# Performance work log

Measured on AMD Instinct MI355X. Metric: run time of the kernel, lower is better.

## Reference

```python
import jax, jax.numpy as jnp
import numpy as np

TOP_K = 2

def setup_inputs() -> dict:
    key = jax.random.key(0)
    k0, k1, k2, k3 = jax.random.split(key, 4)
    B, T, D, F, E = 2, 2048, 1024, 4096, 8
    x = jax.random.normal(k0, (B, T, D), dtype=jnp.float32)
    Wr = jax.random.normal(k1, (E, D), dtype=jnp.float32) * 0.02   # router weight [out=E, in=D]
    W1 = jax.random.normal(k2, (E, F, D), dtype=jnp.float32) * 0.02  # per-expert up-proj [out=F, in=D]
    W2 = jax.random.normal(k3, (E, D, F), dtype=jnp.float32) * 0.02  # per-expert down-proj [out=D, in=F]
    return {"x": x, "Wr": Wr, "W1": W1, "W2": W2}

def reference(x, Wr, W1, W2):
    B, T, D = x.shape
    E = Wr.shape[0]
    N = B * T
    xf = x.reshape(N, D)
    # Router in fp32 on the un-cast activations (as in the torch module).
    logits = xf @ Wr.T                                   # [N, E]
    probs = jax.nn.softmax(logits, axis=-1)
    topk_w, topk_idx = jax.lax.top_k(probs, TOP_K)       # [N, K]
    topk_w = topk_w / jnp.sum(topk_w, axis=-1, keepdims=True)
    # Combine weights scattered into a dense [N, E] dispatch/combine matrix
    # (top_k indices are distinct, so .set is exact).
    combine = jnp.zeros((N, E), dtype=jnp.float32)
    combine = combine.at[jnp.arange(N)[:, None], topk_idx].set(topk_w)
    # Expert FFN runs in bf16 (comm_dtype in the original all-to-all pipeline).
    xb = xf.astype(jnp.bfloat16)
    h = jax.nn.gelu(jnp.einsum('nd,efd->enf', xb, W1.astype(jnp.bfloat16)),
                    approximate=False)                   # [E, N, F]
    yo = jnp.einsum('enf,edf->end', h, W2.astype(jnp.bfloat16))  # [E, N, D]
    # Weighted combine: bf16 expert outputs * fp32 gate weights -> fp32 (torch promotion).
    out = jnp.einsum('end,ne->nd', yo.astype(jnp.float32), combine)
    return out.reshape(B, T, D)
```

## Files before the change

kernel.cpp:

```cpp
#include <hip/hip_runtime.h>
#include <hip/hip_bf16.h>

typedef __attribute__((ext_vector_type(8))) __bf16 bf16x8;
typedef __attribute__((ext_vector_type(4))) float floatx4;

constexpr int N_TOK = 4096;
constexpr int DDIM  = 1024;
constexpr int FDIM  = 4096;
constexpr int NEXP  = 8;
constexpr int NSLOT = 2 * N_TOK;

static __device__ __forceinline__ unsigned short f2bf(float f) {
    union { __hip_bfloat16 h; unsigned short u; } v;
    v.h = __float2bfloat16(f);
    return v.u;
}

__global__ void zero_kernel(float* __restrict__ out, int* __restrict__ counts) {
    size_t i = ((size_t)blockIdx.x * 256 + threadIdx.x) * 4;
    *(float4*)(out + i) = make_float4(0.f, 0.f, 0.f, 0.f);
    if (blockIdx.x == 0 && threadIdx.x < NEXP) counts[threadIdx.x] = 0;
}

__global__ void castN_kernel(const float* __restrict__ src, unsigned short* __restrict__ dst, int n4) {
    int i = blockIdx.x * 256 + threadIdx.x;
    if (i >= n4) return;
    float4 v = *(const float4*)(src + (size_t)i * 4);
    ushort4 o;
    o.x = f2bf(v.x); o.y = f2bf(v.y); o.z = f2bf(v.z); o.w = f2bf(v.w);
    *(ushort4*)(dst + (size_t)i * 4) = o;
}

__global__ void router_kernel(const float* __restrict__ x, const float* __restrict__ Wr,
                              int* __restrict__ te, float* __restrict__ tw,
                              int* __restrict__ counts) {
    __shared__ float wr[NEXP * DDIM];
    const int tid = threadIdx.x;
    for (int i = tid; i < NEXP * DDIM; i += 256) wr[i] = Wr[i];
    __syncthreads();
    const int wave = tid >> 6, lane = tid & 63;
    const int t = blockIdx.x * 4 + wave;

    float xr[16];
    const float* xp = x + (size_t)t * DDIM;
    #pragma unroll
    for (int i = 0; i < 16; i++) xr[i] = xp[lane + 64 * i];

    float logit[NEXP];
    #pragma unroll
    for (int e = 0; e < NEXP; e++) {
        float s = 0.f;
        #pragma unroll
        for (int i = 0; i < 16; i++) s += xr[i] * wr[e * DDIM + lane + 64 * i];
        #pragma unroll
        for (int off = 32; off > 0; off >>= 1) s += __shfl_xor(s, off, 64);
        logit[e] = s;
    }
    if (lane == 0) {
        int i0 = 0; float l0 = logit[0];
        #pragma unroll
        for (int e = 1; e < NEXP; e++) if (logit[e] > l0) { l0 = logit[e]; i0 = e; }
        int i1 = -1; float l1 = -3.0e38f;
        #pragma unroll
        for (int e = 0; e < NEXP; e++) if (e != i0 && logit[e] > l1) { l1 = logit[e]; i1 = e; }
        float p1 = __expf(0.f) * expf(l1 - l0);
        float w0 = 1.f / (1.f + p1);
        float w1 = p1 * w0;
        te[t * 2] = i0; te[t * 2 + 1] = i1;
        tw[t * 2] = w0; tw[t * 2 + 1] = w1;
        atomicAdd(&counts[i0], 1);
        atomicAdd(&counts[i1], 1);
    }
}

__global__ void scan_kernel(const int* __restrict__ counts, int* __restrict__ offsets,
                            int* __restrict__ cursors) {
    if (threadIdx.x == 0) {
        int acc = 0;
        for (int e = 0; e < NEXP; e++) { offsets[e] = acc; acc += counts[e]; }
        offsets[NEXP] = acc;
    }
    if (threadIdx.x < NEXP) cursors[threadIdx.x] = 0;
}

__global__ void scatter_kernel(const int* __restrict__ te, const float* __restrict__ tw,
                               const int* __restrict__ offsets, int* __restrict__ cursors,
                               int* __restrict__ rowid, float* __restrict__ gate) {
    int t = blockIdx.x * 256 + threadIdx.x;
    if (t >= N_TOK) return;
    #pragma unroll
    for (int k = 0; k < 2; k++) {
        int e = te[t * 2 + k];
        int pos = atomicAdd(&cursors[e], 1);
        int slot = offsets[e] + pos;
        rowid[slot] = t;
        gate[slot] = tw[t * 2 + k];
    }
}

template <int K, bool UP, bool BF16W>
__global__ __launch_bounds__(256)
void ffn_gemm(const unsigned short* __restrict__ A,
              const float* __restrict__ Wf,
              const unsigned short* __restrict__ Wb,
              unsigned short* __restrict__ Hout,
              float* __restrict__ out,
              const int* __restrict__ rowid,
              const float* __restrict__ gate,
              const int* __restrict__ offsets) {
    constexpr int BM = 128, BN = 128, BK = 32, LDT = 40;
    constexpr int NOUT = UP ? FDIM : DDIM;

    const int e = blockIdx.z;
    const int seg = offsets[e];
    const int cnt = offsets[e + 1] - seg;
    const int m0 = blockIdx.y * BM;
    if (m0 >= cnt) return;
    const int n0 = blockIdx.x * BN;

    __shared__ __align__(16) unsigned short As[BM * LDT];
    __shared__ __align__(16) unsigned short Bs[BN * LDT];

    const int tid = threadIdx.x;
    const int lane = tid & 63;
    const int wave = tid >> 6;
    const int wm = (wave >> 1) * 64;
    const int wn = (wave & 1) * 64;
    const int frow = lane & 15;
    const int quad = lane >> 4;

    floatx4 acc[4][4];
    #pragma unroll
    for (int i = 0; i < 4; i++)
        #pragma unroll
        for (int j = 0; j < 4; j++)
            acc[i][j] = (floatx4){0.f, 0.f, 0.f, 0.f};

    const int ar = tid >> 1;
    const int ah = (tid & 1) * 16;

    int slotA = seg + m0 + ar;
    if (slotA > NSLOT - 1) slotA = NSLOT - 1;
    const unsigned short* aptr;
    if (UP) aptr = A + (size_t)rowid[slotA] * DDIM + ah;
    else    aptr = A + (size_t)slotA * FDIM + ah;
    unsigned short* asdst = &As[ar * LDT + ah];
    unsigned short* bsdst = &Bs[ar * LDT + ah];
    const float* bptrf = Wf + ((size_t)e * NOUT + n0 + ar) * K + ah;
    const unsigned short* bptrb = Wb + ((size_t)e * NOUT + n0 + ar) * K + ah;

    for (int k0 = 0; k0 < K; k0 += BK) {
        uint4 a0 = *(const uint4*)(aptr);
        uint4 a1 = *(const uint4*)(aptr + 8);
        uint4 bu0, bu1;
        if (BF16W) {
            bu0 = *(const uint4*)(bptrb);
            bu1 = *(const uint4*)(bptrb + 8);
        } else {
            float4 b0 = *(const float4*)(bptrf);
            float4 b1 = *(const float4*)(bptrf + 4);
            float4 b2 = *(const float4*)(bptrf + 8);
            float4 b3 = *(const float4*)(bptrf + 12);
            union { unsigned short u[16]; uint4 q[2]; } bb;
            bb.u[0] = f2bf(b0.x); bb.u[1] = f2bf(b0.y); bb.u[2]  = f2bf(b0.z); bb.u[3]  = f2bf(b0.w);
            bb.u[4] = f2bf(b1.x); bb.u[5] = f2bf(b1.y); bb.u[6]  = f2bf(b1.z); bb.u[7]  = f2bf(b1.w);
            bb.u[8] = f2bf(b2.x); bb.u[9] = f2bf(b2.y); bb.u[10] = f2bf(b2.z); bb.u[11] = f2bf(b2.w);
            bb.u[12] = f2bf(b3.x); bb.u[13] = f2bf(b3.y); bb.u[14] = f2bf(b3.z); bb.u[15] = f2bf(b3.w);
            bu0 = bb.q[0]; bu1 = bb.q[1];
        }
        __syncthreads();
        *(uint4*)(asdst) = a0;
        *(uint4*)(asdst + 8) = a1;
        *(uint4*)(bsdst) = bu0;
        *(uint4*)(bsdst + 8) = bu1;
        __syncthreads();

        bf16x8 av[4], bv[4];
        #pragma unroll
        for (int i = 0; i < 4; i++)
            av[i] = *(const bf16x8*)&As[(wm + i * 16 + frow) * LDT + quad * 8];
        #pragma unroll
        for (int i = 0; i < 4; i++)
            bv[i] = *(const bf16x8*)&Bs[(wn + i * 16 + frow) * LDT + quad * 8];
        #pragma unroll
        for (int mt = 0; mt < 4; mt++)
            #pragma unroll
            for (int nt = 0; nt < 4; nt++)
                acc[mt][nt] = __builtin_amdgcn_mfma_f32_16x16x32_bf16(av[mt], bv[nt], acc[mt][nt], 0, 0, 0);

        aptr += BK;
        if (BF16W) bptrb += BK; else bptrf += BK;
    }

    #pragma unroll
    for (int mt = 0; mt < 4; mt++) {
        #pragma unroll
        for (int r = 0; r < 4; r++) {
            int mloc = m0 + wm + mt * 16 + quad * 4 + r;
            if (mloc >= cnt) continue;
            int slot = seg + mloc;
            if (UP) {
                #pragma unroll
                for (int nt = 0; nt < 4; nt++) {
                    int n = n0 + wn + nt * 16 + frow;
                    float v = acc[mt][nt][r];
                    float g = 0.5f * v * (1.0f + erff(v * 0.70710678118654752f));
                    Hout[(size_t)slot * FDIM + n] = f2bf(g);
                }
            } else {
                int t = rowid[slot];
                float gw = gate[slot];
                #pragma unroll
                for (int nt = 0; nt < 4; nt++) {
                    int n = n0 + wn + nt * 16 + frow;
                    atomicAdd(&out[(size_t)t * DDIM + n], gw * acc[mt][nt][r]);
                }
            }
        }
    }
}

extern "C" void kernel_launch(void* const* d_in, const int* in_sizes, int n_in,
                              void* d_out, int out_size, void* d_ws, size_t ws_size,
                              hipStream_t stream) {
    const float* x  = (const float*)d_in[0];
    const float* Wr = (const float*)d_in[1];
    const float* W1 = (const float*)d_in[2];
    const float* W2 = (const float*)d_in[3];
    float* out = (float*)d_out;

    char* ws = (char*)d_ws;
    size_t off = 0;
    auto alloc = [&](size_t bytes) -> char* {
        char* p = ws + off;
        off = (off + bytes + 255) & ~(size_t)255;
        return p;
    };
    unsigned short* xb   = (unsigned short*)alloc((size_t)N_TOK * DDIM * 2);
    unsigned short* H    = (unsigned short*)alloc((size_t)NSLOT * FDIM * 2);
    int*   rowid   = (int*)alloc(NSLOT * 4);
    float* gatew   = (float*)alloc(NSLOT * 4);
    int*   te      = (int*)alloc(NSLOT * 4);
    float* tw      = (float*)alloc(NSLOT * 4);
    int*   counts  = (int*)alloc(64);
    int*   offsets = (int*)alloc(64);
    int*   cursors = (int*)alloc(64);
    unsigned short* w1b = (unsigned short*)alloc((size_t)NEXP * FDIM * DDIM * 2);
    unsigned short* w2b = (unsigned short*)alloc((size_t)NEXP * DDIM * FDIM * 2);
    const bool bf16w = (off <= ws_size);

    zero_kernel<<<4096, 256, 0, stream>>>(out, counts);
    castN_kernel<<<(N_TOK * DDIM / 4 + 255) / 256, 256, 0, stream>>>(x, xb, N_TOK * DDIM / 4);
    if (bf16w) {
        const int n4 = NEXP * FDIM * DDIM / 4;
        castN_kernel<<<(n4 + 255) / 256, 256, 0, stream>>>(W1, w1b, n4);
        castN_kernel<<<(n4 + 255) / 256, 256, 0, stream>>>(W2, w2b, n4);
    }
    router_kernel<<<N_TOK / 4, 256, 0, stream>>>(x, Wr, te, tw, counts);
    scan_kernel<<<1, 64, 0, stream>>>(counts, offsets, cursors);
    scatter_kernel<<<(N_TOK + 255) / 256, 256, 0, stream>>>(te, tw, offsets, cursors, rowid, gatew);

    if (bf16w) {
        ffn_gemm<DDIM, true,  true ><<<dim3(FDIM / 128, 32, NEXP), 256, 0, stream>>>(xb, W1, w1b, H, out, rowid, gatew, offsets);
        ffn_gemm<FDIM, false, true ><<<dim3(DDIM / 128, 32, NEXP), 256, 0, stream>>>(H,  W2, w2b, H, out, rowid, gatew, offsets);
    } else {
        ffn_gemm<DDIM, true,  false><<<dim3(FDIM / 128, 32, NEXP), 256, 0, stream>>>(xb, W1, w1b, H, out, rowid, gatew, offsets);
        ffn_gemm<FDIM, false, false><<<dim3(DDIM / 128, 32, NEXP), 256, 0, stream>>>(H,  W2, w2b, H, out, rowid, gatew, offsets);
    }
}
```

Measured before the change: 732.0 us.

## Load GEMM tiles with direct global-to-LDS and replace atomic combine with slot buffer

```diff
diff --git a/kernel.cpp b/kernel.cpp
--- a/kernel.cpp
+++ b/kernel.cpp
@@ -16,9 +16,20 @@
     return v.u;
 }
 
-__global__ void zero_kernel(float* __restrict__ out, int* __restrict__ counts) {
-    size_t i = ((size_t)blockIdx.x * 256 + threadIdx.x) * 4;
-    *(float4*)(out + i) = make_float4(0.f, 0.f, 0.f, 0.f);
+static __device__ __forceinline__ void gl2lds16(const unsigned short* g, unsigned short* l) {
+    __builtin_amdgcn_global_load_lds(
+        (__attribute__((address_space(1))) void*)g,
+        (__attribute__((address_space(3))) void*)l,
+        16, 0, 0);
+}
+
+__global__ void castX_kernel(const float* __restrict__ src, unsigned short* __restrict__ dst,
+                             int* __restrict__ counts) {
+    int i = blockIdx.x * 256 + threadIdx.x;
+    float4 v = *(const float4*)(src + (size_t)i * 4);
+    ushort4 o;
+    o.x = f2bf(v.x); o.y = f2bf(v.y); o.z = f2bf(v.z); o.w = f2bf(v.w);
+    *(ushort4*)(dst + (size_t)i * 4) = o;
     if (blockIdx.x == 0 && threadIdx.x < NEXP) counts[threadIdx.x] = 0;
 }
 
@@ -63,7 +74,7 @@
         int i1 = -1; float l1 = -3.0e38f;
         #pragma unroll
         for (int e = 0; e < NEXP; e++) if (e != i0 && logit[e] > l1) { l1 = logit[e]; i1 = e; }
-        float p1 = __expf(0.f) * expf(l1 - l0);
+        float p1 = expf(l1 - l0);
         float w0 = 1.f / (1.f + p1);
         float w1 = p1 * w0;
         te[t * 2] = i0; te[t * 2 + 1] = i1;
@@ -85,7 +96,8 @@
 
 __global__ void scatter_kernel(const int* __restrict__ te, const float* __restrict__ tw,
                                const int* __restrict__ offsets, int* __restrict__ cursors,
-                               int* __restrict__ rowid, float* __restrict__ gate) {
+                               int* __restrict__ rowid, float* __restrict__ gate,
+                               int* __restrict__ tok2slot) {
     int t = blockIdx.x * 256 + threadIdx.x;
     if (t >= N_TOK) return;
     #pragma unroll
@@ -95,6 +107,7 @@
         int slot = offsets[e] + pos;
         rowid[slot] = t;
         gate[slot] = tw[t * 2 + k];
+        tok2slot[t * 2 + k] = slot;
     }
 }
 
@@ -104,11 +117,11 @@
               const float* __restrict__ Wf,
               const unsigned short* __restrict__ Wb,
               unsigned short* __restrict__ Hout,
-              float* __restrict__ out,
+              float* __restrict__ Y,
               const int* __restrict__ rowid,
               const float* __restrict__ gate,
               const int* __restrict__ offsets) {
-    constexpr int BM = 128, BN = 128, BK = 32, LDT = 40;
+    constexpr int BM = 128, BN = 128, BK = 32, LDT = 32;
     constexpr int NOUT = UP ? FDIM : DDIM;
 
     const int e = blockIdx.z;
@@ -124,6 +137,38 @@
     const int tid = threadIdx.x;
     const int lane = tid & 63;
     const int wave = tid >> 6;
+
+    const int srow0 = wave * 32 + (lane >> 2);
+    const int chunk = lane & 3;
+
+    const unsigned short* ag[2];
+    #pragma unroll
+    for (int j = 0; j < 2; j++) {
+        int r = srow0 + j * 16;
+        int slot = seg + m0 + r;
+        if (slot >= NSLOT) slot = NSLOT - 1;
+        if (UP) { int t = rowid[slot]; ag[j] = A + (size_t)t * DDIM + chunk * 8; }
+        else    { ag[j] = A + (size_t)slot * FDIM + chunk * 8; }
+    }
+    const unsigned short* bg[2];
+    #pragma unroll
+    for (int j = 0; j < 2; j++) {
+        int r = srow0 + j * 16;
+        bg[j] = Wb + ((size_t)e * NOUT + n0 + r) * K + chunk * 8;
+    }
+    unsigned short* asl[2];
+    unsigned short* bsl[2];
+    #pragma unroll
+    for (int j = 0; j < 2; j++) {
+        asl[j] = &As[(wave * 32 + j * 16) * LDT] + lane * 8;
+        bsl[j] = &Bs[(wave * 32 + j * 16) * LDT] + lane * 8;
+    }
+
+    const int br = tid >> 1;
+    const int bh = (tid & 1) * 16;
+    const float* bptrf = Wf + ((size_t)e * NOUT + n0 + br) * K + bh;
+    unsigned short* bsdst = &Bs[br * LDT + bh];
+
     const int wm = (wave >> 1) * 64;
     const int wn = (wave & 1) * 64;
     const int frow = lane & 15;
@@ -136,27 +181,9 @@
         for (int j = 0; j < 4; j++)
             acc[i][j] = (floatx4){0.f, 0.f, 0.f, 0.f};
 
-    const int ar = tid >> 1;
-    const int ah = (tid & 1) * 16;
-
-    int slotA = seg + m0 + ar;
-    if (slotA > NSLOT - 1) slotA = NSLOT - 1;
-    const unsigned short* aptr;
-    if (UP) aptr = A + (size_t)rowid[slotA] * DDIM + ah;
-    else    aptr = A + (size_t)slotA * FDIM + ah;
-    unsigned short* asdst = &As[ar * LDT + ah];
-    unsigned short* bsdst = &Bs[ar * LDT + ah];
-    const float* bptrf = Wf + ((size_t)e * NOUT + n0 + ar) * K + ah;
-    const unsigned short* bptrb = Wb + ((size_t)e * NOUT + n0 + ar) * K + ah;
-
     for (int k0 = 0; k0 < K; k0 += BK) {
-        uint4 a0 = *(const uint4*)(aptr);
-        uint4 a1 = *(const uint4*)(aptr + 8);
         uint4 bu0, bu1;
-        if (BF16W) {
-            bu0 = *(const uint4*)(bptrb);
-            bu1 = *(const uint4*)(bptrb + 8);
-        } else {
+        if (!BF16W) {
             float4 b0 = *(const float4*)(bptrf);
             float4 b1 = *(const float4*)(bptrf + 4);
             float4 b2 = *(const float4*)(bptrf + 8);
@@ -167,12 +194,20 @@
             bb.u[8] = f2bf(b2.x); bb.u[9] = f2bf(b2.y); bb.u[10] = f2bf(b2.z); bb.u[11] = f2bf(b2.w);
             bb.u[12] = f2bf(b3.x); bb.u[13] = f2bf(b3.y); bb.u[14] = f2bf(b3.z); bb.u[15] = f2bf(b3.w);
             bu0 = bb.q[0]; bu1 = bb.q[1];
+            bptrf += BK;
         }
         __syncthreads();
-        *(uint4*)(asdst) = a0;
-        *(uint4*)(asdst + 8) = a1;
-        *(uint4*)(bsdst) = bu0;
-        *(uint4*)(bsdst + 8) = bu1;
+        gl2lds16(ag[0], asl[0]);
+        gl2lds16(ag[1], asl[1]);
+        if (BF16W) {
+            gl2lds16(bg[0], bsl[0]);
+            gl2lds16(bg[1], bsl[1]);
+            bg[0] += BK; bg[1] += BK;
+        } else {
+            *(uint4*)(bsdst) = bu0;
+            *(uint4*)(bsdst + 8) = bu1;
+        }
+        ag[0] += BK; ag[1] += BK;
         __syncthreads();
 
         bf16x8 av[4], bv[4];
@@ -187,9 +222,6 @@
             #pragma unroll
             for (int nt = 0; nt < 4; nt++)
                 acc[mt][nt] = __builtin_amdgcn_mfma_f32_16x16x32_bf16(av[mt], bv[nt], acc[mt][nt], 0, 0, 0);
-
-        aptr += BK;
-        if (BF16W) bptrb += BK; else bptrf += BK;
     }
 
     #pragma unroll
@@ -208,16 +240,27 @@
                     Hout[(size_t)slot * FDIM + n] = f2bf(g);
                 }
             } else {
-                int t = rowid[slot];
                 float gw = gate[slot];
                 #pragma unroll
                 for (int nt = 0; nt < 4; nt++) {
                     int n = n0 + wn + nt * 16 + frow;
-                    atomicAdd(&out[(size_t)t * DDIM + n], gw * acc[mt][nt][r]);
+                    Y[(size_t)slot * DDIM + n] = gw * acc[mt][nt][r];
                 }
             }
         }
     }
+}
+
+__global__ void combine_kernel(const float* __restrict__ Y, const int* __restrict__ tok2slot,
+                               float* __restrict__ out) {
+    int idx = blockIdx.x * 256 + threadIdx.x;
+    int t = idx >> 8;
+    int c = (idx & 255) * 4;
+    int s0 = tok2slot[t * 2], s1 = tok2slot[t * 2 + 1];
+    float4 a = *(const float4*)(Y + (size_t)s0 * DDIM + c);
+    float4 b = *(const float4*)(Y + (size_t)s1 * DDIM + c);
+    *(float4*)(out + (size_t)t * DDIM + c) =
+        make_float4(a.x + b.x, a.y + b.y, a.z + b.z, a.w + b.w);
 }
 
 extern "C" void kernel_launch(void* const* d_in, const int* in_sizes, int n_in,
@@ -238,10 +281,12 @@
     };
     unsigned short* xb   = (unsigned short*)alloc((size_t)N_TOK * DDIM * 2);
     unsigned short* H    = (unsigned short*)alloc((size_t)NSLOT * FDIM * 2);
+    float* Yb      = (float*)alloc((size_t)NSLOT * DDIM * 4);
     int*   rowid   = (int*)alloc(NSLOT * 4);
     float* gatew   = (float*)alloc(NSLOT * 4);
     int*   te      = (int*)alloc(NSLOT * 4);
     float* tw      = (float*)alloc(NSLOT * 4);
+    int*   t2s     = (int*)alloc(NSLOT * 4);
     int*   counts  = (int*)alloc(64);
     int*   offsets = (int*)alloc(64);
     int*   cursors = (int*)alloc(64);
@@ -249,8 +294,7 @@
     unsigned short* w2b = (unsigned short*)alloc((size_t)NEXP * DDIM * FDIM * 2);
     const bool bf16w = (off <= ws_size);
 
-    zero_kernel<<<4096, 256, 0, stream>>>(out, counts);
-    castN_kernel<<<(N_TOK * DDIM / 4 + 255) / 256, 256, 0, stream>>>(x, xb, N_TOK * DDIM / 4);
+    castX_kernel<<<N_TOK * DDIM / 4 / 256, 256, 0, stream>>>(x, xb, counts);
     if (bf16w) {
         const int n4 = NEXP * FDIM * DDIM / 4;
         castN_kernel<<<(n4 + 255) / 256, 256, 0, stream>>>(W1, w1b, n4);
@@ -258,13 +302,14 @@
     }
     router_kernel<<<N_TOK / 4, 256, 0, stream>>>(x, Wr, te, tw, counts);
     scan_kernel<<<1, 64, 0, stream>>>(counts, offsets, cursors);
-    scatter_kernel<<<(N_TOK + 255) / 256, 256, 0, stream>>>(te, tw, offsets, cursors, rowid, gatew);
+    scatter_kernel<<<(N_TOK + 255) / 256, 256, 0, stream>>>(te, tw, offsets, cursors, rowid, gatew, t2s);
 
     if (bf16w) {
-        ffn_gemm<DDIM, true,  true ><<<dim3(FDIM / 128, 32, NEXP), 256, 0, stream>>>(xb, W1, w1b, H, out, rowid, gatew, offsets);
-        ffn_gemm<FDIM, false, true ><<<dim3(DDIM / 128, 32, NEXP), 256, 0, stream>>>(H,  W2, w2b, H, out, rowid, gatew, offsets);
+        ffn_gemm<DDIM, true,  true ><<<dim3(FDIM / 128, 32, NEXP), 256, 0, stream>>>(xb, W1, w1b, H, Yb, rowid, gatew, offsets);
+        ffn_gemm<FDIM, false, true ><<<dim3(DDIM / 128, 32, NEXP), 256, 0, stream>>>(H,  W2, w2b, H, Yb, rowid, gatew, offsets);
     } else {
-        ffn_gemm<DDIM, true,  false><<<dim3(FDIM / 128, 32, NEXP), 256, 0, stream>>>(xb, W1, w1b, H, out, rowid, gatew, offsets);
-        ffn_gemm<FDIM, false, false><<<dim3(DDIM / 128, 32, NEXP), 256, 0, stream>>>(H,  W2, w2b, H, out, rowid, gatew, offsets);
-    }
-}
+        ffn_gemm<DDIM, true,  false><<<dim3(FDIM / 128, 32, NEXP), 256, 0, stream>>>(xb, W1, w1b, H, Yb, rowid, gatew, offsets);
+        ffn_gemm<FDIM, false, false><<<dim3(DDIM / 128, 32, NEXP), 256, 0, stream>>>(H,  W2, w2b, H, Yb, rowid, gatew, offsets);
+    }
+    combine_kernel<<<N_TOK, 256, 0, stream>>>(Yb, t2s, out);
+}
```

New measurement: 698.5 us. -4.6%, faster.
